# Performance work log

Measured on AMD Instinct MI355X. Metric: run time of the kernel, lower is better.

Reference implementation:

```python
import jax, jax.numpy as jnp
import numpy as np

B, T, C, H = 2, 2048, 1024, 16
DH = C // H
EPS = 1e-5


def _rotary(t_len, d_head):
    inv_freq = 1.0 / (10000.0 ** (jnp.arange(0, d_head, 2, dtype=jnp.float32) / d_head))
    t = jnp.arange(t_len, dtype=jnp.float32)
    freqs = t[:, None] * inv_freq[None, :]           # [T, dh/2]
    emb = jnp.concatenate([freqs, freqs], axis=-1)    # [T, dh]
    return jnp.cos(emb), jnp.sin(emb)


def _apply_rope(x, cos, sin):
    # x: [B,H,T,dh]; cos/sin: [T,dh]
    d = x.shape[-1]
    x1, x2 = x[..., : d // 2], x[..., d // 2 :]
    x_rot = jnp.concatenate([-x2, x1], axis=-1)
    return x * cos + x_rot * sin


def _decay_mask(t_len, n_head):
    gammas = 1.0 - 2.0 ** (-5.0 - jnp.arange(n_head, dtype=jnp.float32))  # [H]
    n = jnp.arange(t_len)[:, None]
    m = jnp.arange(t_len)[None, :]
    dist = n - m
    decay = gammas[:, None, None] ** jnp.maximum(dist, 0).astype(jnp.float32)
    return jnp.where(dist[None] >= 0, decay, 0.0)  # [H,T,T]


def setup_inputs() -> dict:
    key = jax.random.key(0)
    ks = jax.random.split(key, 7)
    s = 1.0 / np.sqrt(C)
    return {
        "x": jax.random.normal(ks[0], (B, T, C), dtype=jnp.float32),
        "Wq": jax.random.normal(ks[1], (C, C), dtype=jnp.float32) * s,
        "Wk": jax.random.normal(ks[2], (C, C), dtype=jnp.float32) * s,
        "Wv": jax.random.normal(ks[3], (C, C), dtype=jnp.float32) * s,
        "Wo": jax.random.normal(ks[4], (C, C), dtype=jnp.float32) * s,
        "gn_weight": jnp.ones((C,), dtype=jnp.float32),
        "gn_bias": jnp.zeros((C,), dtype=jnp.float32),
    }


def reference(x, Wq, Wk, Wv, Wo, gn_weight, gn_bias):
    b, t, c = x.shape
    # projections (torch Linear: y = x @ W.T), split heads -> [B,H,T,dh]
    def proj(W):
        return jnp.einsum("btc,oc->bto", x, W).reshape(b, t, H, DH).transpose(0, 2, 1, 3)
    q, k, v = proj(Wq), proj(Wk), proj(Wv)

    cos, sin = _rotary(t, DH)
    q = _apply_rope(q, cos, sin)
    k = _apply_rope(k, cos, sin)

    decay = _decay_mask(t, H)                          # [H,T,T]
    qk = jnp.einsum("bhtd,bhsd->bhts", q, k) * (1.0 / np.sqrt(DH))
    qk = qk * decay[None]
    out = jnp.einsum("bhts,bhsd->bhtd", qk, v)         # [B,H,T,dh]

    # GroupNorm with n_head groups over channels, per token
    out = out.transpose(0, 2, 1, 3)                    # [B,T,H,dh]
    mu = jnp.mean(out, axis=-1, keepdims=True)
    var = jnp.mean((out - mu) ** 2, axis=-1, keepdims=True)
    out = (out - mu) * jax.lax.rsqrt(var + EPS)
    out = out * gn_weight.reshape(H, DH) + gn_bias.reshape(H, DH)

    out = out.reshape(b, t, c)
    return jnp.einsum("btc,oc->bto", out, Wo)
```

## Files before the change

### kernel.cpp

```cpp
#include <hip/hip_runtime.h>
#include <stdint.h>

#define B_ 2
#define T_ 2048
#define C_ 1024
#define H_ 16
#define DH_ 64
#define M_ (B_*T_)

typedef short bhalf8 __attribute__((ext_vector_type(8)));
typedef float floatx4 __attribute__((ext_vector_type(4)));

__device__ __forceinline__ short f2bf(float f) {
  unsigned u = __float_as_uint(f);
  u += 0x7fffu + ((u >> 16) & 1u);
  return (short)(u >> 16);
}
__device__ __forceinline__ float bf2f(short s) {
  return __uint_as_float(((unsigned)(unsigned short)s) << 16);
}

__device__ __forceinline__ void gll16(void* lds_dst, const void* g_src) {
  __builtin_amdgcn_global_load_lds(
      reinterpret_cast<const uint32_t __attribute__((address_space(1)))*>(
          reinterpret_cast<uintptr_t>(g_src)),
      reinterpret_cast<uint32_t __attribute__((address_space(3)))*>(
          reinterpret_cast<uintptr_t>(lds_dst)),
      16, 0, 0);
}

__global__ void cvt_all(
    const float* __restrict__ x,  const float* __restrict__ wq,
    const float* __restrict__ wk, const float* __restrict__ wv,
    const float* __restrict__ wo,
    short* __restrict__ xb, short* __restrict__ wqb, short* __restrict__ wkb,
    short* __restrict__ wvb, short* __restrict__ wob)
{
  int i = blockIdx.x * blockDim.x + threadIdx.x;
  const float* s; short* d; int off;
  if (i < (M_*C_/4)) { s = x; d = xb; off = i; }
  else {
    int j = i - M_*C_/4;
    int w = j >> 18;
    off = j & ((1<<18) - 1);
    s = (w==0) ? wq : (w==1) ? wk : (w==2) ? wv : wo;
    d = (w==0) ? wqb : (w==1) ? wkb : (w==2) ? wvb : wob;
  }
  float4 v = ((const float4*)s)[off];
  short4 o;
  o.x = f2bf(v.x); o.y = f2bf(v.y); o.z = f2bf(v.z); o.w = f2bf(v.w);
  ((short4*)d)[off] = o;
}

__global__ __launch_bounds__(512, 2) void gemm_qkv(
    const short* __restrict__ X,
    const short* __restrict__ Wq, const short* __restrict__ Wk, const short* __restrict__ Wv,
    short* __restrict__ Qb, short* __restrict__ Kb, short* __restrict__ Vt,
    short* __restrict__ Kt)
{
  __shared__ __align__(16) short SM[4*256*64];
  short (*As)[256*64] = (short (*)[256*64])(SM);
  short (*Bs)[256*64] = (short (*)[256*64])(SM + 2*256*64);
  short* Ct = SM;

  const int tid  = threadIdx.x;
  const int lane = tid & 63;
  const int wid  = tid >> 6;
  const int l15  = lane & 15;
  const int quad = lane >> 4;
  const int wr   = wid >> 2;
  const int wc   = wid & 3;
  const int K    = C_;

  const int bid = blockIdx.x;
  const int wg  = (bid & 7) * 24 + (bid >> 3);
  const int nx  = wg % 12;
  const int m0  = (wg / 12) << 8;

  int kind, nloc;
  const short *Ab, *Bb;
  if (nx < 4)      { kind = 0; nloc = nx << 8;       Ab = X  + (size_t)m0*K;   Bb = Wq + (size_t)nloc*K; }
  else if (nx < 8) { kind = 1; nloc = (nx - 4) << 8; Ab = X  + (size_t)m0*K;   Bb = Wk + (size_t)nloc*K; }
  else             { kind = 2; nloc = (nx - 8) << 8; Ab = Wv + (size_t)nloc*K; Bb = X  + (size_t)m0*K;   }

  const int r_loc = tid >> 3;
  const int g_lin = tid & 7;

  auto stageU = [&](short* lds, const short* g, int q, int k0) {
    int row = (q << 6) + r_loc;
    int gs  = g_lin ^ (row & 7);
    gll16(lds + (q << 12) + (wid << 9), g + (size_t)row * K + k0 + (gs << 3));
  };

  floatx4 acc[8][4] = {};

  stageU(&Bs[0][0], Bb, 0, 0); stageU(&Bs[0][0], Bb, 1, 0);
  stageU(&Bs[0][0], Bb, 2, 0); stageU(&Bs[0][0], Bb, 3, 0);
  stageU(&As[0][0], Ab, 0, 0); stageU(&As[0][0], Ab, 2, 0);
  stageU(&As[0][0], Ab, 1, 0); stageU(&As[0][0], Ab, 3, 0);
  asm volatile("s_waitcnt vmcnt(2)" ::: "memory");
  __builtin_amdgcn_s_barrier();
  __builtin_amdgcn_sched_barrier(0);

  for (int t = 0; t < 16; ++t) {
    const int buf = t & 1, nbuf = buf ^ 1;
    const int kn = (t + 1) << 6;
    const bool pf = (t < 15);
    bhalf8 aF[4], bF[4];

#pragma unroll
    for (int i = 0; i < 4; ++i) {
      int row = (wr << 7) + (i << 4) + l15;
      aF[i] = *(const bhalf8*)&As[buf][(row << 6) + ((quad ^ (row & 7)) << 3)];
    }
#pragma unroll
    for (int n = 0; n < 4; ++n) {
      int row = (wc << 6) + (n << 4) + l15;
      bF[n] = *(const bhalf8*)&Bs[buf][(row << 6) + ((quad ^ (row & 7)) << 3)];
    }
    if (pf) { stageU(&Bs[nbuf][0], Bb, 0, kn); stageU(&Bs[nbuf][0], Bb, 1, kn); }
    __builtin_amdgcn_s_barrier();
    asm volatile("s_waitcnt lgkmcnt(0)" ::: "memory");
    __builtin_amdgcn_sched_barrier(0);
    __builtin_amdgcn_s_setprio(1);
#pragma unroll
    for (int i = 0; i < 4; ++i)
#pragma unroll
      for (int n = 0; n < 4; ++n)
        acc[i][n] = __builtin_amdgcn_mfma_f32_16x16x32_bf16(aF[i], bF[n], acc[i][n], 0, 0, 0);
    __builtin_amdgcn_s_setprio(0);
    asm volatile("s_waitcnt vmcnt(2)" ::: "memory");
    __builtin_amdgcn_s_barrier();
    __builtin_amdgcn_sched_barrier(0);

#pragma unroll
    for (int i = 0; i < 4; ++i) {
      int row = (wr << 7) + ((4 + i) << 4) + l15;
      aF[i] = *(const bhalf8*)&As[buf][(row << 6) + ((quad ^ (row & 7)) << 3)];
    }
    if (pf) { stageU(&Bs[nbuf][0], Bb, 2, kn); stageU(&Bs[nbuf][0], Bb, 3, kn); }
    __builtin_amdgcn_s_barrier();
    asm volatile("s_waitcnt lgkmcnt(0)" ::: "memory");
    __builtin_amdgcn_sched_barrier(0);
    __builtin_amdgcn_s_setprio(1);
#pragma unroll
    for (int i = 0; i < 4; ++i)
#pragma unroll
      for (int n = 0; n < 4; ++n)
        acc[4 + i][n] = __builtin_amdgcn_mfma_f32_16x16x32_bf16(aF[i], bF[n], acc[4 + i][n], 0, 0, 0);
    __builtin_amdgcn_s_setprio(0);
    asm volatile("s_waitcnt vmcnt(4)" ::: "memory");
    __builtin_amdgcn_s_barrier();
    __builtin_amdgcn_sched_barrier(0);

#pragma unroll
    for (int i = 0; i < 4; ++i) {
      int row = (wr << 7) + (i << 4) + l15;
      aF[i] = *(const bhalf8*)&As[buf][(row << 6) + (((4 + quad) ^ (row & 7)) << 3)];
    }
#pragma unroll
    for (int n = 0; n < 4; ++n) {
      int row = (wc << 6) + (n << 4) + l15;
      bF[n] = *(const bhalf8*)&Bs[buf][(row << 6) + (((4 + quad) ^ (row & 7)) << 3)];
    }
    if (pf) { stageU(&As[nbuf][0], Ab, 0, kn); stageU(&As[nbuf][0], Ab, 2, kn); }
    __builtin_amdgcn_s_barrier();
    asm volatile("s_waitcnt lgkmcnt(0)" ::: "memory");
    __builtin_amdgcn_sched_barrier(0);
    __builtin_amdgcn_s_setprio(1);
#pragma unroll
    for (int i = 0; i < 4; ++i)
#pragma unroll
      for (int n = 0; n < 4; ++n)
        acc[i][n] = __builtin_amdgcn_mfma_f32_16x16x32_bf16(aF[i], bF[n], acc[i][n], 0, 0, 0);
    __builtin_amdgcn_s_setprio(0);
    asm volatile("s_waitcnt vmcnt(6)" ::: "memory");
    __builtin_amdgcn_s_barrier();
    __builtin_amdgcn_sched_barrier(0);

#pragma unroll
    for (int i = 0; i < 4; ++i) {
      int row = (wr << 7) + ((4 + i) << 4) + l15;
      aF[i] = *(const bhalf8*)&As[buf][(row << 6) + (((4 + quad) ^ (row & 7)) << 3)];
    }
    if (pf) { stageU(&As[nbuf][0], Ab, 1, kn); stageU(&As[nbuf][0], Ab, 3, kn); }
    __builtin_amdgcn_s_barrier();
    asm volatile("s_waitcnt lgkmcnt(0)" ::: "memory");
    __builtin_amdgcn_sched_barrier(0);
    __builtin_amdgcn_s_setprio(1);
#pragma unroll
    for (int i = 0; i < 4; ++i)
#pragma unroll
      for (int n = 0; n < 4; ++n)
        acc[4 + i][n] = __builtin_amdgcn_mfma_f32_16x16x32_bf16(aF[i], bF[n], acc[4 + i][n], 0, 0, 0);
    __builtin_amdgcn_s_setprio(0);
    asm volatile("s_waitcnt vmcnt(2)" ::: "memory");
    __builtin_amdgcn_s_barrier();
    __builtin_amdgcn_sched_barrier(0);
  }

  if (kind < 2) {
    short* Cb = kind ? Kb : Qb;
    const int hh = (nloc + (wc << 6)) >> 6;
    const float frq0 = exp2f((float)l15        * (-0.4152410118609203f));
    const float frq1 = exp2f((float)(l15 + 16) * (-0.4152410118609203f));
    const int swz = (l15 & 7) << 3;
#pragma unroll
    for (int m = 0; m < 8; ++m)
#pragma unroll
      for (int r = 0; r < 4; ++r) {
        int tl = (wr << 7) + (m << 4) + (quad << 2) + r;
        int n  = m0 + tl;
        int bb = n >> 11, tt = n & (T_ - 1);
        size_t base = ((size_t)(bb * H_ + hh) * T_ + tt) * DH_;
        float tf = (float)tt;
        float v0, v1, v2, v3;
        {
          float ang = tf * frq0;
          float sn = __sinf(ang), cs = __cosf(ang);
          float xlo = acc[m][0][r], xhi = acc[m][2][r];
          v0 = xlo * cs - xhi * sn;
          v1 = xhi * cs + xlo * sn;
          Cb[base + l15]      = f2bf(v0);
          Cb[base + l15 + 32] = f2bf(v1);
        }
        {
          float ang = tf * frq1;
          float sn = __sinf(ang), cs = __cosf(ang);
          float xlo = acc[m][1][r], xhi = acc[m][3][r];
          v2 = xlo * cs - xhi * sn;
          v3 = xhi * cs + xlo * sn;
          Cb[base + l15 + 16] = f2bf(v2);
          Cb[base + l15 + 48] = f2bf(v3);
        }
        if (kind == 1) {
          int tswz = tl ^ swz;
          int cb = (wc << 6);
          Ct[(cb + l15)      * 256 + tswz] = f2bf(v0);
          Ct[(cb + l15 + 32) * 256 + tswz] = f2bf(v1);
          Ct[(cb + l15 + 16) * 256 + tswz] = f2bf(v2);
          Ct[(cb + l15 + 48) * 256 + tswz] = f2bf(v3);
        }
      }
    if (kind == 1) {
      __syncthreads();
      const int hb = nloc >> 6;
#pragma unroll
      for (int rr = 0; rr < 16; ++rr) {
        int lin = rr * 512 + tid;
        int cc_ = lin >> 5;
        int g   = lin & 31;
        bhalf8 v = *(const bhalf8*)&Ct[cc_ * 256 + ((g ^ (cc_ & 7)) << 3)];
        int tg = m0 + (g << 3);
        int bb = tg >> 11, tt = tg & (T_ - 1);
        size_t dst = ((size_t)(bb * H_ + hb + (cc_ >> 6)) * DH_ + (cc_ & 63)) * T_ + tt;
        *(bhalf8*)&Kt[dst] = v;
      }
    }
  } else {
#pragma unroll
    for (int m = 0; m < 8; ++m)
#pragma unroll
      for (int r = 0; r < 4; ++r) {
        int o = nloc + (wr << 7) + (m << 4) + (quad << 2) + r;
#pragma unroll
        for (int n = 0; n < 4; ++n) {
          int tk = m0 + (wc << 6) + (n << 4) + l15;
          int bb = tk >> 11, tt = tk & (T_ - 1);
          Vt[(size_t)bb * (C_ * T_) + (size_t)o * T_ + tt] = f2bf(acc[m][n][r]);
        }
      }
  }
}

__global__ __launch_bounds__(256) void gemm_out(
    const short* __restrict__ A, const short* __restrict__ Bm, float* __restrict__ Cf)
{
  __shared__ __align__(16) short As[2][128*64];
  __shared__ __align__(16) short Bs[2][64*64];
  const int tid = threadIdx.x, lane = tid & 63, wv = tid >> 6;
  const int l15 = lane & 15, quad = lane >> 4;
  const int n0 = blockIdx.x << 6;
  const int m0 = blockIdx.y << 7;

  const short* Ab = A  + (size_t)m0 * C_;
  const short* Bb = Bm + (size_t)n0 * C_;

  auto stage = [&](int buf, int k0) {
#pragma unroll
    for (int i = 0; i < 4; ++i) {
      int slot = (i<<8) + tid, r = slot >> 3, g = (slot & 7) ^ (r & 7);
      gll16(&As[buf][((i<<8) + (wv<<6))*8], Ab + (size_t)r*C_ + k0 + (g<<3));
    }
#pragma unroll
    for (int i = 0; i < 2; ++i) {
      int slot = (i<<8) + tid, r = slot >> 3, g = (slot & 7) ^ (r & 7);
      gll16(&Bs[buf][((i<<8) + (wv<<6))*8], Bb + (size_t)r*C_ + k0 + (g<<3));
    }
  };

  floatx4 acc[2][4] = {};
  stage(0, 0);
  int cur = 0;
  for (int it = 0; it < 16; ++it) {
    __syncthreads();
    if (it < 15) stage(cur ^ 1, (it + 1) << 6);
    bhalf8 af[2][2], bfr[2][4];
#pragma unroll
    for (int ks = 0; ks < 2; ++ks) {
#pragma unroll
      for (int rt = 0; rt < 2; ++rt) {
        int row = (wv<<5) + rt*16 + l15;
        af[ks][rt] = *(const bhalf8*)&As[cur][(row<<6) + ((((ks<<2)+quad) ^ (row&7))<<3)];
      }
#pragma unroll
      for (int ct = 0; ct < 4; ++ct) {
        int row = ct*16 + l15;
        bfr[ks][ct] = *(const bhalf8*)&Bs[cur][(row<<6) + ((((ks<<2)+quad) ^ (row&7))<<3)];
      }
    }
#pragma unroll
    for (int ks = 0; ks < 2; ++ks)
#pragma unroll
      for (int rt = 0; rt < 2; ++rt)
#pragma unroll
        for (int ct = 0; ct < 4; ++ct)
          acc[rt][ct] = __builtin_amdgcn_mfma_f32_16x16x32_bf16(af[ks][rt], bfr[ks][ct], acc[rt][ct], 0, 0, 0);
    cur ^= 1;
  }

#pragma unroll
  for (int rt = 0; rt < 2; ++rt)
#pragma unroll
    for (int r = 0; r < 4; ++r) {
      int n = m0 + (wv<<5) + rt*16 + quad*4 + r;
#pragma unroll
      for (int ct = 0; ct < 4; ++ct)
        Cf[(size_t)n * C_ + n0 + ct*16 + l15] = acc[rt][ct][r];
    }
}

__global__ __launch_bounds__(256) void seg_state(
    const short* __restrict__ Kt, const short* __restrict__ Vt,
    short* __restrict__ Pseg)
{
  __shared__ __align__(16) short Ks[2][64*64];
  __shared__ __align__(16) short Vs[2][64*64];
  const int tid = threadIdx.x, lane = tid & 63, wv = tid >> 6;
  const int l15 = lane & 15, quad = lane >> 4;
  const int wrow = wv << 4;
  const int bh = blockIdx.x >> 3, p = blockIdx.x & 7;
  const int h = bh & 15;
  const float log2g = log2f(1.f - exp2f(-5.f - (float)h));
  const float g64 = exp2f(log2g * 64.f);

  float wgt[16];
#pragma unroll
  for (int ks = 0; ks < 2; ++ks)
#pragma unroll
    for (int i = 0; i < 8; ++i)
      wgt[ks*8 + i] = exp2f(log2g * (float)(64 - (ks*32 + (quad<<3) + i)));

  const short* Ktg = Kt + (size_t)bh*DH_*T_;
  const short* Vtg = Vt + (size_t)bh*DH_*T_;

  auto stage = [&](int buf, int jc) {
    const int m0 = ((p<<2) + jc) << 6;
#pragma unroll
    for (int i = 0; i < 2; ++i) {
      int slot = (i<<8) + tid;
      int r = slot >> 3, g = (slot & 7) ^ (r & 7);
      gll16(&Ks[buf][((i<<8) + (wv<<6))*8], Ktg + (size_t)r*T_ + m0 + (g<<3));
      gll16(&Vs[buf][((i<<8) + (wv<<6))*8], Vtg + (size_t)r*T_ + m0 + (g<<3));
    }
  };

  floatx4 acc[4] = {};
  stage(0, 0);
  int cur = 0;
  for (int j = 0; j < 4; ++j) {
    __syncthreads();
    if (j < 3) stage(cur ^ 1, j + 1);
#pragma unroll
    for (int ct = 0; ct < 4; ++ct)
#pragma unroll
      for (int r = 0; r < 4; ++r) acc[ct][r] *= g64;
#pragma unroll
    for (int ks = 0; ks < 2; ++ks) {
      int row = wrow + l15;
      bhalf8 va = *(const bhalf8*)&Vs[cur][(row<<6) + ((((ks<<2)+quad) ^ (row&7))<<3)];
      bhalf8 aw;
#pragma unroll
      for (int i = 0; i < 8; ++i) aw[i] = f2bf(bf2f(va[i]) * wgt[ks*8 + i]);
      bhalf8 bk[4];
#pragma unroll
      for (int ct = 0; ct < 4; ++ct) {
        int kr = ct*16 + l15;
        bk[ct] = *(const bhalf8*)&Ks[cur][(kr<<6) + ((((ks<<2)+quad) ^ (kr&7))<<3)];
      }
#pragma unroll
      for (int ct = 0; ct < 4; ++ct)
        acc[ct] = __builtin_amdgcn_mfma_f32_16x16x32_bf16(aw, bk[ct], acc[ct], 0, 0, 0);
    }
    cur ^= 1;
  }
  size_t base = (size_t)(bh*8 + p) * 2 * 4096;
#pragma unroll
  for (int ct = 0; ct < 4; ++ct)
#pragma unroll
    for (int r = 0; r < 4; ++r) {
      int e = wrow + (quad<<2) + r, d = ct*16 + l15;
      float x = acc[ct][r];
      short hi = f2bf(x);
      short lo = f2bf(x - bf2f(hi));
      Pseg[base + e*64 + d]        = hi;
      Pseg[base + 4096 + e*64 + d] = lo;
    }
}

__global__ __launch_bounds__(256) void retention_chunk(
    const short* __restrict__ Qb, const short* __restrict__ Kb,
    const short* __restrict__ Kt, const short* __restrict__ Vt,
    const short* __restrict__ Pseg,
    const float* __restrict__ gnw, const float* __restrict__ gnb,
    short* __restrict__ Xn)
{
  __shared__ __align__(16) short Vs[64*64];
  __shared__ __align__(16) short Kts[64*64];
  __shared__ __align__(16) short KSs[64*64];
  __shared__ __align__(16) short Sh[64*64];
  __shared__ __align__(16) short Sl[64*64];

  const int tid = threadIdx.x, lane = tid & 63, wv = tid >> 6;
  const int l15 = lane & 15, quad = lane >> 4;
  const int wrow = wv << 4;

  const int idx = blockIdx.x;
  const int bh = idx & 31;
  const int cc = idx >> 5;
  const int c  = ((cc & 7) << 2) | (cc >> 3);
  const int p = c >> 2, j = c & 3;
  const int b = bh >> 4, h = bh & 15;
  const int n0 = c << 6;

  const float log2g = log2f(1.f - exp2f(-5.f - (float)h));
  const float g64 = exp2f(log2g * 64.f);

  const short* Qg  = Qb + ((size_t)bh*T_ + n0 + wrow) * DH_;
  const short* Kg  = Kb + (size_t)bh*T_*DH_;
  const short* Ktg = Kt + (size_t)bh*DH_*T_;
  const short* Vtg = Vt + (size_t)bh*DH_*T_;

  bhalf8 aq[2];
#pragma unroll
  for (int ks = 0; ks < 2; ++ks)
    aq[ks] = *(const bhalf8*)(Qg + (size_t)l15*DH_ + ks*32 + quad*8);

  float rowf[4], colf0[4];
#pragma unroll
  for (int r = 0; r < 4; ++r)
    rowf[r] = exp2f(log2g * (float)(wrow + (quad<<2) + r)) * 0.125f;
#pragma unroll
  for (int ct = 0; ct < 4; ++ct)
    colf0[ct] = exp2f(-log2g * (float)(ct*16 + l15));

  const bool has_state = (c > 0);

  floatx4 st[4] = {};
  if (j > 0) {
    float wgt[16];
#pragma unroll
    for (int ks = 0; ks < 2; ++ks)
#pragma unroll
      for (int i = 0; i < 8; ++i)
        wgt[ks*8 + i] = exp2f(log2g * (float)(64 - (ks*32 + (quad<<3) + i)));
    for (int jp = 0; jp < j; ++jp) {
      if (log2g * (float)((j - 1 - jp) << 6) < -34.f) continue;
      const int m0 = ((p<<2) + jp) << 6;
      __syncthreads();
#pragma unroll
      for (int i = 0; i < 2; ++i) {
        int slot = (i<<8) + tid;
        int r = slot >> 3, g = (slot & 7) ^ (r & 7);
        gll16(&Kts[((i<<8) + (wv<<6))*8], Ktg + (size_t)r*T_ + m0 + (g<<3));
        gll16(&Vs[((i<<8) + (wv<<6))*8],  Vtg + (size_t)r*T_ + m0 + (g<<3));
      }
      __syncthreads();
#pragma unroll
      for (int ct = 0; ct < 4; ++ct)
#pragma unroll
        for (int r = 0; r < 4; ++r) st[ct][r] *= g64;
#pragma unroll
      for (int ks = 0; ks < 2; ++ks) {
        int row = wrow + l15;
        bhalf8 va = *(const bhalf8*)&Vs[(row<<6) + ((((ks<<2)+quad) ^ (row&7))<<3)];
        bhalf8 aw;
#pragma unroll
        for (int i = 0; i < 8; ++i) aw[i] = f2bf(bf2f(va[i]) * wgt[ks*8 + i]);
        bhalf8 bk[4];
#pragma unroll
        for (int ct = 0; ct < 4; ++ct) {
          int kr = ct*16 + l15;
          bk[ct] = *(const bhalf8*)&Kts[(kr<<6) + ((((ks<<2)+quad) ^ (kr&7))<<3)];
        }
#pragma unroll
        for (int ct = 0; ct < 4; ++ct)
          st[ct] = __builtin_amdgcn_mfma_f32_16x16x32_bf16(aw, bk[ct], st[ct], 0, 0, 0);
      }
    }
  }
  for (int pp = 0; pp < p; ++pp) {
    float wexp = log2g * (float)(n0 - ((pp + 1) << 8));
    if (wexp < -34.f) continue;
    float w = exp2f(wexp);
    const short* Pg = Pseg + (size_t)(bh*8 + pp) * 2 * 4096;
#pragma unroll
    for (int ct = 0; ct < 4; ++ct)
#pragma unroll
      for (int r = 0; r < 4; ++r) {
        int e = wrow + (quad<<2) + r, d = ct*16 + l15;
        st[ct][r] += w * (bf2f(Pg[e*64 + d]) + bf2f(Pg[4096 + e*64 + d]));
      }
  }
  if (has_state) {
#pragma unroll
    for (int ct = 0; ct < 4; ++ct)
#pragma unroll
      for (int r = 0; r < 4; ++r) {
        int e = wrow + (quad<<2) + r, d = ct*16 + l15;
        float x = st[ct][r];
        short hi = f2bf(x);
        short lo = f2bf(x - bf2f(hi));
        int addr = (e<<6) + ((((d>>3) ^ (e&7))<<3)) + (d&7);
        Sh[addr] = hi; Sl[addr] = lo;
      }
  }

  __syncthreads();
#pragma unroll
  for (int i = 0; i < 2; ++i) {
    int slot = (i<<8) + tid;
    int r = slot >> 3, g = (slot & 7) ^ (r & 7);
    gll16(&KSs[((i<<8) + (wv<<6))*8], Kg  + (size_t)(n0 + r)*DH_ + (g<<3));
    gll16(&Vs[((i<<8) + (wv<<6))*8],  Vtg + (size_t)r*T_ + n0 + (g<<3));
  }
  __syncthreads();

  floatx4 sacc[4] = {};
#pragma unroll
  for (int ks = 0; ks < 2; ++ks) {
    bhalf8 bk[4];
#pragma unroll
    for (int ct = 0; ct < 4; ++ct) {
      int row = ct*16 + l15;
      bk[ct] = *(const bhalf8*)&KSs[(row<<6) + ((((ks<<2)+quad) ^ (row&7))<<3)];
    }
#pragma unroll
    for (int ct = 0; ct < 4; ++ct)
      sacc[ct] = __builtin_amdgcn_mfma_f32_16x16x32_bf16(aq[ks], bk[ct], sacc[ct], 0, 0, 0);
  }
  __syncthreads();
#pragma unroll
  for (int ct = 0; ct < 4; ++ct) {
    float cf = colf0[ct];
    int colg = (ct<<1) + (l15>>3);
    int m = ct*16 + l15;
#pragma unroll
    for (int r = 0; r < 4; ++r) {
      int row = wrow + (quad<<2) + r;
      float v = (row >= m) ? sacc[ct][r] * (rowf[r] * cf) : 0.f;
      KSs[(row<<6) + ((colg ^ ((row>>1)&7))<<3) + (l15&7)] = f2bf(v);
    }
  }
  floatx4 oacc[4] = {};
#pragma unroll
  for (int ks = 0; ks < 2; ++ks) {
    int row = wrow + l15;
    bhalf8 as_ = *(const bhalf8*)&KSs[(row<<6) + ((((ks<<2)+quad) ^ ((row>>1)&7))<<3)];
    bhalf8 bv[4];
#pragma unroll
    for (int ct = 0; ct < 4; ++ct) {
      int vrow = ct*16 + l15;
      bv[ct] = *(const bhalf8*)&Vs[(vrow<<6) + ((((ks<<2)+quad) ^ (vrow&7))<<3)];
    }
#pragma unroll
    for (int ct = 0; ct < 4; ++ct)
      oacc[ct] = __builtin_amdgcn_mfma_f32_16x16x32_bf16(as_, bv[ct], oacc[ct], 0, 0, 0);
  }

  if (has_state) {
    floatx4 iacc[4] = {};
#pragma unroll
    for (int ks = 0; ks < 2; ++ks) {
      bhalf8 bhf[4], blf[4];
#pragma unroll
      for (int ct = 0; ct < 4; ++ct) {
        int er = ct*16 + l15;
        int ga = ((((ks<<2)+quad) ^ (er&7))<<3);
        bhf[ct] = *(const bhalf8*)&Sh[(er<<6) + ga];
        blf[ct] = *(const bhalf8*)&Sl[(er<<6) + ga];
      }
#pragma unroll
      for (int ct = 0; ct < 4; ++ct) {
        iacc[ct] = __builtin_amdgcn_mfma_f32_16x16x32_bf16(aq[ks], bhf[ct], iacc[ct], 0, 0, 0);
        iacc[ct] = __builtin_amdgcn_mfma_f32_16x16x32_bf16(aq[ks], blf[ct], iacc[ct], 0, 0, 0);
      }
    }
#pragma unroll
    for (int ct = 0; ct < 4; ++ct)
#pragma unroll
      for (int r = 0; r < 4; ++r)
        oacc[ct][r] += rowf[r] * iacc[ct][r];
  }

#pragma unroll
  for (int r = 0; r < 4; ++r) {
    float s1 = oacc[0][r] + oacc[1][r] + oacc[2][r] + oacc[3][r];
    float s2 = oacc[0][r]*oacc[0][r] + oacc[1][r]*oacc[1][r]
             + oacc[2][r]*oacc[2][r] + oacc[3][r]*oacc[3][r];
#pragma unroll
    for (int off = 1; off < 16; off <<= 1) {
      s1 += __shfl_xor(s1, off);
      s2 += __shfl_xor(s2, off);
    }
    float mean = s1 * (1.f/64.f);
    float var  = s2 * (1.f/64.f) - mean*mean;
    float rstd = rsqrtf(var + 1e-5f);
    int t = n0 + wrow + (quad<<2) + r;
    size_t obase = ((size_t)b*T_ + t)*C_ + h*DH_;
#pragma unroll
    for (int ct = 0; ct < 4; ++ct) {
      int d = ct*16 + l15;
      float y = (oacc[ct][r] - mean)*rstd*gnw[h*DH_ + d] + gnb[h*DH_ + d];
      Xn[obase + d] = f2bf(y);
    }
  }
}

extern "C" void kernel_launch(void* const* d_in, const int* in_sizes, int n_in,
                              void* d_out, int out_size, void* d_ws, size_t ws_size,
                              hipStream_t stream) {
  (void)in_sizes; (void)n_in; (void)out_size; (void)ws_size;
  const float* x   = (const float*)d_in[0];
  const float* Wq  = (const float*)d_in[1];
  const float* Wk  = (const float*)d_in[2];
  const float* Wv  = (const float*)d_in[3];
  const float* Wo  = (const float*)d_in[4];
  const float* gnw = (const float*)d_in[5];
  const float* gnb = (const float*)d_in[6];
  float* out = (float*)d_out;

  char* ws = (char*)d_ws;
  short* Xb   = (short*)(ws);
  short* Wqb  = (short*)(ws + (8u<<20));
  short* Pseg = (short*)(ws + (8u<<20));
  short* Wkb  = (short*)(ws + (10u<<20));
  short* Wvb  = (short*)(ws + (12u<<20));
  short* Wob  = (short*)(ws + (14u<<20));
  short* Qb   = (short*)(ws + (16u<<20));
  short* Kb   = (short*)(ws + (24u<<20));
  short* Vtw  = (short*)(ws + (32u<<20));
  short* Xn   = (short*)(ws + (40u<<20));
  short* Ktb  = (short*)(ws + (48u<<20));

  cvt_all<<<(M_*C_/4 + 4*(C_*C_/4)) / 256, 256, 0, stream>>>(
      x, Wq, Wk, Wv, Wo, Xb, Wqb, Wkb, Wvb, Wob);

  gemm_qkv<<<dim3(192), 512, 0, stream>>>(Xb, Wqb, Wkb, Wvb, Qb, Kb, Vtw, Ktb);
  seg_state<<<256, 256, 0, stream>>>(Ktb, Vtw, Pseg);
  retention_chunk<<<1024, 256, 0, stream>>>(Qb, Kb, Ktb, Vtw, Pseg, gnw, gnb, Xn);
  gemm_out<<<dim3(16, 32), 256, 0, stream>>>(Xn, Wob, out);
}
```

Baseline: 165.5 us.

## Precompute per-chunk KV states in seg_state and triple-buffer gemm_out

seg_state now writes each 64-token chunk's K^T V contribution (as hi/lo bf16 pairs) to a new workspace buffer. retention_chunk then sums those precomputed chunk states instead of recomputing intra-segment prefix states with MFMAs. The diagonal K/V tile load is moved to the start of retention_chunk so it overlaps with the Q loads and state accumulation. gemm_out switches to a three-stage LDS pipeline with explicit waitcnt/barrier scheduling and raised priority around the MFMAs; this adds workspace traffic and more LDS per block.

```diff
diff --git a/kernel.cpp b/kernel.cpp
--- a/kernel.cpp
+++ b/kernel.cpp
@@ -276,8 +276,8 @@
 __global__ __launch_bounds__(256) void gemm_out(
     const short* __restrict__ A, const short* __restrict__ Bm, float* __restrict__ Cf)
 {
-  __shared__ __align__(16) short As[2][128*64];
-  __shared__ __align__(16) short Bs[2][64*64];
+  __shared__ __align__(16) short As[3][128*64];
+  __shared__ __align__(16) short Bs[3][64*64];
   const int tid = threadIdx.x, lane = tid & 63, wv = tid >> 6;
   const int l15 = lane & 15, quad = lane >> 4;
   const int n0 = blockIdx.x << 6;
@@ -301,10 +301,13 @@
 
   floatx4 acc[2][4] = {};
   stage(0, 0);
+  stage(1, 64);
+  asm volatile("s_waitcnt vmcnt(6)" ::: "memory");
+  __builtin_amdgcn_s_barrier();
+  __builtin_amdgcn_sched_barrier(0);
+
   int cur = 0;
   for (int it = 0; it < 16; ++it) {
-    __syncthreads();
-    if (it < 15) stage(cur ^ 1, (it + 1) << 6);
     bhalf8 af[2][2], bfr[2][4];
 #pragma unroll
     for (int ks = 0; ks < 2; ++ks) {
@@ -319,6 +322,15 @@
         bfr[ks][ct] = *(const bhalf8*)&Bs[cur][(row<<6) + ((((ks<<2)+quad) ^ (row&7))<<3)];
       }
     }
+    const bool pf = (it < 14);
+    if (pf) {
+      int nb = cur + 2; if (nb >= 3) nb -= 3;
+      stage(nb, (it + 2) << 6);
+    }
+    __builtin_amdgcn_s_barrier();
+    asm volatile("s_waitcnt lgkmcnt(0)" ::: "memory");
+    __builtin_amdgcn_sched_barrier(0);
+    __builtin_amdgcn_s_setprio(1);
 #pragma unroll
     for (int ks = 0; ks < 2; ++ks)
 #pragma unroll
@@ -326,7 +338,12 @@
 #pragma unroll
         for (int ct = 0; ct < 4; ++ct)
           acc[rt][ct] = __builtin_amdgcn_mfma_f32_16x16x32_bf16(af[ks][rt], bfr[ks][ct], acc[rt][ct], 0, 0, 0);
-    cur ^= 1;
+    __builtin_amdgcn_s_setprio(0);
+    if (pf) { asm volatile("s_waitcnt vmcnt(6)" ::: "memory"); }
+    else    { asm volatile("s_waitcnt vmcnt(0)" ::: "memory"); }
+    __builtin_amdgcn_s_barrier();
+    __builtin_amdgcn_sched_barrier(0);
+    if (++cur == 3) cur = 0;
   }
 
 #pragma unroll
@@ -342,7 +359,7 @@
 
 __global__ __launch_bounds__(256) void seg_state(
     const short* __restrict__ Kt, const short* __restrict__ Vt,
-    short* __restrict__ Pseg)
+    short* __restrict__ Pseg, short* __restrict__ Pc)
 {
   __shared__ __align__(16) short Ks[2][64*64];
   __shared__ __align__(16) short Vs[2][64*64];
@@ -381,10 +398,7 @@
   for (int j = 0; j < 4; ++j) {
     __syncthreads();
     if (j < 3) stage(cur ^ 1, j + 1);
-#pragma unroll
-    for (int ct = 0; ct < 4; ++ct)
-#pragma unroll
-      for (int r = 0; r < 4; ++r) acc[ct][r] *= g64;
+    floatx4 pc[4] = {};
 #pragma unroll
     for (int ks = 0; ks < 2; ++ks) {
       int row = wrow + l15;
@@ -400,7 +414,25 @@
       }
 #pragma unroll
       for (int ct = 0; ct < 4; ++ct)
-        acc[ct] = __builtin_amdgcn_mfma_f32_16x16x32_bf16(aw, bk[ct], acc[ct], 0, 0, 0);
+        pc[ct] = __builtin_amdgcn_mfma_f32_16x16x32_bf16(aw, bk[ct], pc[ct], 0, 0, 0);
+    }
+#pragma unroll
+    for (int ct = 0; ct < 4; ++ct)
+#pragma unroll
+      for (int r = 0; r < 4; ++r) acc[ct][r] = acc[ct][r]*g64 + pc[ct][r];
+    if (j < 3) {
+      size_t cbase = (size_t)((bh<<5) + (p<<2) + j) * 2 * 4096;
+#pragma unroll
+      for (int ct = 0; ct < 4; ++ct)
+#pragma unroll
+        for (int r = 0; r < 4; ++r) {
+          int e = wrow + (quad<<2) + r, d = ct*16 + l15;
+          float x = pc[ct][r];
+          short hi = f2bf(x);
+          short lo = f2bf(x - bf2f(hi));
+          Pc[cbase + e*64 + d]        = hi;
+          Pc[cbase + 4096 + e*64 + d] = lo;
+        }
     }
     cur ^= 1;
   }
@@ -420,13 +452,12 @@
 
 __global__ __launch_bounds__(256) void retention_chunk(
     const short* __restrict__ Qb, const short* __restrict__ Kb,
-    const short* __restrict__ Kt, const short* __restrict__ Vt,
-    const short* __restrict__ Pseg,
+    const short* __restrict__ Vt,
+    const short* __restrict__ Pc, const short* __restrict__ Pseg,
     const float* __restrict__ gnw, const float* __restrict__ gnb,
     short* __restrict__ Xn)
 {
   __shared__ __align__(16) short Vs[64*64];
-  __shared__ __align__(16) short Kts[64*64];
   __shared__ __align__(16) short KSs[64*64];
   __shared__ __align__(16) short Sh[64*64];
   __shared__ __align__(16) short Sl[64*64];
@@ -444,13 +475,19 @@
   const int n0 = c << 6;
 
   const float log2g = log2f(1.f - exp2f(-5.f - (float)h));
-  const float g64 = exp2f(log2g * 64.f);
-
-  const short* Qg  = Qb + ((size_t)bh*T_ + n0 + wrow) * DH_;
+
   const short* Kg  = Kb + (size_t)bh*T_*DH_;
-  const short* Ktg = Kt + (size_t)bh*DH_*T_;
   const short* Vtg = Vt + (size_t)bh*DH_*T_;
 
+#pragma unroll
+  for (int i = 0; i < 2; ++i) {
+    int slot = (i<<8) + tid;
+    int r = slot >> 3, g = (slot & 7) ^ (r & 7);
+    gll16(&KSs[((i<<8) + (wv<<6))*8], Kg  + (size_t)(n0 + r)*DH_ + (g<<3));
+    gll16(&Vs[((i<<8) + (wv<<6))*8],  Vtg + (size_t)r*T_ + n0 + (g<<3));
+  }
+
+  const short* Qg = Qb + ((size_t)bh*T_ + n0 + wrow) * DH_;
   bhalf8 aq[2];
 #pragma unroll
   for (int ks = 0; ks < 2; ++ks)
@@ -467,47 +504,18 @@
   const bool has_state = (c > 0);
 
   floatx4 st[4] = {};
-  if (j > 0) {
-    float wgt[16];
-#pragma unroll
-    for (int ks = 0; ks < 2; ++ks)
-#pragma unroll
-      for (int i = 0; i < 8; ++i)
-        wgt[ks*8 + i] = exp2f(log2g * (float)(64 - (ks*32 + (quad<<3) + i)));
-    for (int jp = 0; jp < j; ++jp) {
-      if (log2g * (float)((j - 1 - jp) << 6) < -34.f) continue;
-      const int m0 = ((p<<2) + jp) << 6;
-      __syncthreads();
-#pragma unroll
-      for (int i = 0; i < 2; ++i) {
-        int slot = (i<<8) + tid;
-        int r = slot >> 3, g = (slot & 7) ^ (r & 7);
-        gll16(&Kts[((i<<8) + (wv<<6))*8], Ktg + (size_t)r*T_ + m0 + (g<<3));
-        gll16(&Vs[((i<<8) + (wv<<6))*8],  Vtg + (size_t)r*T_ + m0 + (g<<3));
-      }
-      __syncthreads();
-#pragma unroll
-      for (int ct = 0; ct < 4; ++ct)
-#pragma unroll
-        for (int r = 0; r < 4; ++r) st[ct][r] *= g64;
-#pragma unroll
-      for (int ks = 0; ks < 2; ++ks) {
-        int row = wrow + l15;
-        bhalf8 va = *(const bhalf8*)&Vs[(row<<6) + ((((ks<<2)+quad) ^ (row&7))<<3)];
-        bhalf8 aw;
-#pragma unroll
-        for (int i = 0; i < 8; ++i) aw[i] = f2bf(bf2f(va[i]) * wgt[ks*8 + i]);
-        bhalf8 bk[4];
-#pragma unroll
-        for (int ct = 0; ct < 4; ++ct) {
-          int kr = ct*16 + l15;
-          bk[ct] = *(const bhalf8*)&Kts[(kr<<6) + ((((ks<<2)+quad) ^ (kr&7))<<3)];
-        }
-#pragma unroll
-        for (int ct = 0; ct < 4; ++ct)
-          st[ct] = __builtin_amdgcn_mfma_f32_16x16x32_bf16(aw, bk[ct], st[ct], 0, 0, 0);
-      }
-    }
+  for (int jp = 0; jp < j; ++jp) {
+    float wexp = log2g * (float)((j - 1 - jp) << 6);
+    if (wexp < -34.f) continue;
+    float w = exp2f(wexp);
+    const short* Pg = Pc + (size_t)((bh<<5) + (p<<2) + jp) * 2 * 4096;
+#pragma unroll
+    for (int ct = 0; ct < 4; ++ct)
+#pragma unroll
+      for (int r = 0; r < 4; ++r) {
+        int e = wrow + (quad<<2) + r, d = ct*16 + l15;
+        st[ct][r] += w * (bf2f(Pg[e*64 + d]) + bf2f(Pg[4096 + e*64 + d]));
+      }
   }
   for (int pp = 0; pp < p; ++pp) {
     float wexp = log2g * (float)(n0 - ((pp + 1) << 8));
@@ -536,14 +544,6 @@
       }
   }
 
-  __syncthreads();
-#pragma unroll
-  for (int i = 0; i < 2; ++i) {
-    int slot = (i<<8) + tid;
-    int r = slot >> 3, g = (slot & 7) ^ (r & 7);
-    gll16(&KSs[((i<<8) + (wv<<6))*8], Kg  + (size_t)(n0 + r)*DH_ + (g<<3));
-    gll16(&Vs[((i<<8) + (wv<<6))*8],  Vtg + (size_t)r*T_ + n0 + (g<<3));
-  }
   __syncthreads();
 
   floatx4 sacc[4] = {};
@@ -662,12 +662,13 @@
   short* Vtw  = (short*)(ws + (32u<<20));
   short* Xn   = (short*)(ws + (40u<<20));
   short* Ktb  = (short*)(ws + (48u<<20));
+  short* Pcb  = (short*)(ws + (64u<<20));
 
   cvt_all<<<(M_*C_/4 + 4*(C_*C_/4)) / 256, 256, 0, stream>>>(
       x, Wq, Wk, Wv, Wo, Xb, Wqb, Wkb, Wvb, Wob);
 
   gemm_qkv<<<dim3(192), 512, 0, stream>>>(Xb, Wqb, Wkb, Wvb, Qb, Kb, Vtw, Ktb);
-  seg_state<<<256, 256, 0, stream>>>(Ktb, Vtw, Pseg);
-  retention_chunk<<<1024, 256, 0, stream>>>(Qb, Kb, Ktb, Vtw, Pseg, gnw, gnb, Xn);
+  seg_state<<<256, 256, 0, stream>>>(Ktb, Vtw, Pseg, Pcb);
+  retention_chunk<<<1024, 256, 0, stream>>>(Qb, Kb, Vtw, Pcb, Pseg, gnw, gnb, Xn);
   gemm_out<<<dim3(16, 32), 256, 0, stream>>>(Xn, Wob, out);
 }
```

Result: no change. 166.9 us (+0.9%).
